# Kernel optimization log

Measured on AMD Instinct MI355X. Metric: run time of the kernel, lower is better.

## Reference

```python
import jax, jax.numpy as jnp
import numpy as np

EPS_BN = 1e-5
EPS_ATTN = 1e-9


def bn(h, g, b, m, v):
    # inference-mode BatchNorm1d over channel (last) dim
    return (h - m) * (g * jax.lax.rsqrt(v + EPS_BN)) + b


def setup_inputs() -> dict:
    key = jax.random.key(0)
    ks = jax.random.split(key, 16)
    B, N, Cin, C = 16, 2048, 64, 256
    std = 0.05
    inp = {
        "x": jax.random.normal(ks[0], (B, N, Cin), jnp.float32),
        "w1": jax.random.normal(ks[1], (C, Cin), jnp.float32) * std,
        "w2": jax.random.normal(ks[2], (C, C), jnp.float32) * std,
        "wqk": jax.random.normal(ks[3], (C, C), jnp.float32) * std,
        "wv": jax.random.normal(ks[4], (C, C), jnp.float32) * std,
        "bv": jax.random.normal(ks[5], (C,), jnp.float32) * std,
        "wt": jax.random.normal(ks[6], (C, C), jnp.float32) * std,
        "bt": jax.random.normal(ks[7], (C,), jnp.float32) * std,
    }
    for i, name in enumerate(["bn1", "bn2", "bn3"]):
        k = jax.random.split(ks[8 + i], 4)
        inp[name + "_g"] = 1.0 + 0.1 * jax.random.normal(k[0], (C,), jnp.float32)
        inp[name + "_b"] = 0.1 * jax.random.normal(k[1], (C,), jnp.float32)
        inp[name + "_m"] = 0.1 * jax.random.normal(k[2], (C,), jnp.float32)
        inp[name + "_v"] = jax.random.uniform(k[3], (C,), jnp.float32, 0.5, 1.5)
    return inp


def reference(x, w1, w2, wqk, wv, bv, wt, bt,
              bn1_g, bn1_b, bn1_m, bn1_v,
              bn2_g, bn2_b, bn2_m, bn2_v,
              bn3_g, bn3_b, bn3_m, bn3_v):
    # x: [B, N, Cin]; all feature maps kept channel-last [B, N, C]
    h = jax.nn.relu(bn(jnp.einsum('bnc,dc->bnd', x, w1), bn1_g, bn1_b, bn1_m, bn1_v))
    h = jax.nn.relu(bn(jnp.einsum('bnc,dc->bnd', h, w2), bn2_g, bn2_b, bn2_m, bn2_v))

    # SA_Layer: q and k share the same (bias-free) 1x1 conv weights
    q = jnp.einsum('bnc,dc->bnd', h, wqk)          # [B,N,C]
    energy = jnp.einsum('bic,bjc->bij', q, q)      # [B,N,N]
    attn = jax.nn.softmax(energy, axis=-1)
    attn = attn / (EPS_ATTN + jnp.sum(attn, axis=1, keepdims=True))  # L1 renorm over queries
    v = jnp.einsum('bnc,dc->bnd', h, wv) + bv      # [B,N,C]
    x_r = jnp.einsum('bic,bij->bjc', v, attn)      # [B,N,C]

    t = jnp.einsum('bnc,dc->bnd', h - x_r, wt) + bt
    t = jax.nn.relu(bn(t, bn3_g, bn3_b, bn3_m, bn3_v))
    out = h + t                                    # [B,N,C]
    return jnp.transpose(out, (0, 2, 1))           # [B,C,N] as in torch module
```

## Files before the change

### kernel.cpp

```cpp
#include <hip/hip_runtime.h>
#include <hip/hip_bf16.h>

#define B_  16
#define N_  2048
#define C_  256
#define BN_ (B_*N_)

typedef __bf16 bf16x8 __attribute__((ext_vector_type(8)));
typedef float  f32x4  __attribute__((ext_vector_type(4)));
typedef int    i32x4  __attribute__((ext_vector_type(4)));

static __device__ __forceinline__ f32x4 MFMA(bf16x8 a, bf16x8 b, f32x4 c){
  return __builtin_amdgcn_mfma_f32_16x16x32_bf16(a, b, c, 0, 0, 0);
}
static __device__ __forceinline__ unsigned short f2b(float f){
  unsigned int u = __float_as_uint(f);
  u += 0x7fffu + ((u >> 16) & 1u);
  return (unsigned short)(u >> 16);
}

__global__ void prep_kernel(
    const float* __restrict__ w1, const float* __restrict__ w2,
    const float* __restrict__ wqk, const float* __restrict__ wv,
    const float* __restrict__ bv, const float* __restrict__ wt,
    const float* __restrict__ bt,
    const float* __restrict__ g1, const float* __restrict__ b1,
    const float* __restrict__ m1, const float* __restrict__ v1,
    const float* __restrict__ g2, const float* __restrict__ b2,
    const float* __restrict__ m2, const float* __restrict__ v2,
    const float* __restrict__ g3, const float* __restrict__ b3,
    const float* __restrict__ m3, const float* __restrict__ v3,
    unsigned short* __restrict__ w1b, unsigned short* __restrict__ w2b,
    unsigned short* __restrict__ wqkb, unsigned short* __restrict__ wvb,
    unsigned short* __restrict__ wtb,
    float* __restrict__ bias1, float* __restrict__ bias2,
    float* __restrict__ biasv, float* __restrict__ biast)
{
  const int d = blockIdx.x;
  const int c = threadIdx.x;
  const float s1 = g1[d] * rsqrtf(v1[d] + 1e-5f);
  const float s2 = g2[d] * rsqrtf(v2[d] + 1e-5f);
  const float s3 = g3[d] * rsqrtf(v3[d] + 1e-5f);
  if (c < 64) w1b[d*64 + c] = f2b(w1[d*64 + c] * s1);
  w2b[d*256 + c]  = f2b(w2[d*256 + c] * s2);
  wqkb[d*256 + c] = f2b(wqk[d*256 + c]);
  wvb[d*256 + c]  = f2b(wv[d*256 + c]);
  wtb[d*256 + c]  = f2b(wt[d*256 + c] * s3);
  if (c == 0){
    bias1[d] = b1[d] - m1[d]*s1;
    bias2[d] = b2[d] - m2[d]*s2;
    biasv[d] = bv[d];
    biast[d] = bt[d]*s3 + b3[d] - m3[d]*s3;
  }
}

template<int MODE, int K>
__global__ __launch_bounds__(256, 2) void wgemm(
    const void* __restrict__ inp, const unsigned short* __restrict__ wB,
    const float* __restrict__ bias, const float* __restrict__ hf32,
    void* __restrict__ out0, void* __restrict__ out1)
{
  extern __shared__ char smem[];
  unsigned short* Al = (unsigned short*)smem;
  unsigned short* Bl = (unsigned short*)(smem + 64*72*2);
  const int tid  = threadIdx.x;
  const int lane = tid & 63;
  const int w    = tid >> 6;
  const int wr   = w >> 1, wc = w & 1;
  const long row0 = (long)blockIdx.x * 64;

  f32x4 acc[2][8];
  #pragma unroll
  for (int m = 0; m < 2; ++m)
    #pragma unroll
    for (int n = 0; n < 8; ++n) acc[m][n] = f32x4{0.f,0.f,0.f,0.f};

  const int KS = K / 64;
  #pragma unroll 1
  for (int s = 0; s < KS; ++s){
    if (s) __syncthreads();
    if constexpr (MODE == 0){
      const float* xin = (const float*)inp;
      #pragma unroll
      for (int t = 0; t < 4; ++t){
        int idx = tid + t*256;
        int r = idx >> 4, c4 = (idx & 15) * 4;
        float4 v = *(const float4*)(xin + (row0 + r)*K + c4);
        unsigned short* dst = &Al[r*72 + c4];
        dst[0]=f2b(v.x); dst[1]=f2b(v.y); dst[2]=f2b(v.z); dst[3]=f2b(v.w);
      }
    } else {
      const unsigned short* bin = (const unsigned short*)inp;
      #pragma unroll
      for (int t = 0; t < 2; ++t){
        int idx = tid + t*256;
        int r = idx >> 3, c8 = (idx & 7) * 8;
        *(i32x4*)&Al[r*72 + c8] = *(const i32x4*)(bin + (row0 + r)*K + s*64 + c8);
      }
    }
    #pragma unroll
    for (int t = 0; t < 8; ++t){
      int idx = tid + t*256;
      int d = idx >> 3, c8 = (idx & 7) * 8;
      *(i32x4*)&Bl[d*72 + c8] = *(const i32x4*)(wB + d*K + s*64 + c8);
    }
    __syncthreads();
    #pragma unroll
    for (int kk = 0; kk < 2; ++kk){
      bf16x8 a[2], b[8];
      #pragma unroll
      for (int m = 0; m < 2; ++m)
        a[m] = *(const bf16x8*)&Al[(32*wr + 16*m + (lane&15))*72 + kk*32 + (lane>>4)*8];
      #pragma unroll
      for (int n = 0; n < 8; ++n)
        b[n] = *(const bf16x8*)&Bl[(128*wc + 16*n + (lane&15))*72 + kk*32 + (lane>>4)*8];
      #pragma unroll
      for (int m = 0; m < 2; ++m)
        #pragma unroll
        for (int n = 0; n < 8; ++n)
          acc[m][n] = MFMA(a[m], b[n], acc[m][n]);
    }
  }

  if constexpr (MODE <= 2){
    unsigned short* obf = (unsigned short*)out0;
    float* of = (float*)out1;
    #pragma unroll
    for (int n = 0; n < 8; ++n){
      int col = 128*wc + 16*n + (lane&15);
      float bs = 0.f;
      if constexpr (MODE != 2) bs = bias[col];
      #pragma unroll
      for (int m = 0; m < 2; ++m){
        int rl = 32*wr + 16*m + (lane>>4)*4;
        #pragma unroll
        for (int r = 0; r < 4; ++r){
          float v = acc[m][n][r] + bs;
          if constexpr (MODE == 0 || MODE == 1) v = fmaxf(v, 0.f);
          obf[(row0 + rl + r)*256 + col] = f2b(v);
          if constexpr (MODE == 1) of[(row0 + rl + r)*256 + col] = v;
        }
      }
    }
  } else if constexpr (MODE == 3){
    __syncthreads();
    unsigned short* Vl = (unsigned short*)smem;
    #pragma unroll
    for (int n = 0; n < 8; ++n){
      int col = 128*wc + 16*n + (lane&15);
      float bs = bias[col];
      #pragma unroll
      for (int m = 0; m < 2; ++m){
        int rl = 32*wr + 16*m + (lane>>4)*4;
        #pragma unroll
        for (int r = 0; r < 4; ++r)
          Vl[(rl + r)*264 + col] = f2b(acc[m][n][r] + bs);
      }
    }
    __syncthreads();
    long b = row0 >> 11;
    int  n0 = (int)(row0 & 2047);
    unsigned short* vt = (unsigned short*)out0 + b*(256L*2048);
    #pragma unroll 1
    for (int cc = 0; cc < 64; ++cc){
      int c = 64*w + cc;
      vt[(long)c*2048 + n0 + lane] = Vl[lane*264 + c];
    }
  } else {
    __syncthreads();
    float* Ol = (float*)smem;
    #pragma unroll
    for (int n = 0; n < 8; ++n){
      int col = 128*wc + 16*n + (lane&15);
      float bs = bias[col];
      #pragma unroll
      for (int m = 0; m < 2; ++m){
        int rl = 32*wr + 16*m + (lane>>4)*4;
        #pragma unroll
        for (int r = 0; r < 4; ++r){
          float t = fmaxf(acc[m][n][r] + bs, 0.f);
          float h = hf32[(row0 + rl + r)*256 + col];
          Ol[(rl + r)*265 + col] = h + t;
        }
      }
    }
    __syncthreads();
    long b = row0 >> 11;
    int  n0 = (int)(row0 & 2047);
    float* op = (float*)out0 + b*(256L*2048);
    #pragma unroll 1
    for (int cc = 0; cc < 64; ++cc){
      int c = 64*w + cc;
      op[(long)c*2048 + n0 + lane] = Ol[lane*265 + c];
    }
  }
}

__global__ __launch_bounds__(256, 2) void pass1_kernel(
    const unsigned short* __restrict__ q,
    float* __restrict__ rowm, float* __restrict__ rowl)
{
  __shared__ unsigned short qi[64*264];
  __shared__ float smm[4][64], sml[4][64];
  const int tid = threadIdx.x, lane = tid & 63, w = tid >> 6;
  const int lin = blockIdx.y * 32 + blockIdx.x;
  const int swz = (lin & 7) * 64 + (lin >> 3);
  const int b  = swz >> 5;
  const int i0 = (swz & 31) * 64;
  const unsigned short* qb = q + (long)b*N_*C_;

  #pragma unroll
  for (int t = 0; t < 8; ++t){
    int idx = tid + t*256;
    int r = idx >> 5, c8 = (idx & 31) * 8;
    *(i32x4*)&qi[r*264 + c8] = *(const i32x4*)(qb + (long)(i0 + r)*256 + c8);
  }
  __syncthreads();

  float mr[4][4], lr[4][4];
  #pragma unroll
  for (int i = 0; i < 4; ++i)
    #pragma unroll
    for (int r = 0; r < 4; ++r){ mr[i][r] = -3e38f; lr[i][r] = 0.f; }

  #pragma unroll 1
  for (int js = 0; js < 8; ++js){
    const int j0 = js*256 + 64*w;
    f32x4 e[4][4];
    #pragma unroll
    for (int i = 0; i < 4; ++i)
      #pragma unroll
      for (int j = 0; j < 4; ++j) e[i][j] = f32x4{0.f,0.f,0.f,0.f};

    #pragma unroll
    for (int kk = 0; kk < 8; ++kk){
      bf16x8 a[4], bb[4];
      #pragma unroll
      for (int i = 0; i < 4; ++i)
        a[i] = *(const bf16x8*)&qi[(16*i + (lane&15))*264 + kk*32 + (lane>>4)*8];
      #pragma unroll
      for (int j = 0; j < 4; ++j)
        bb[j] = *(const bf16x8*)(qb + (long)(j0 + 16*j + (lane&15))*256 + kk*32 + (lane>>4)*8);
      #pragma unroll
      for (int i = 0; i < 4; ++i)
        #pragma unroll
        for (int j = 0; j < 4; ++j)
          e[i][j] = MFMA(a[i], bb[j], e[i][j]);
    }
    #pragma unroll
    for (int i = 0; i < 4; ++i)
      #pragma unroll
      for (int r = 0; r < 4; ++r){
        float tm = fmaxf(fmaxf(e[i][0][r], e[i][1][r]), fmaxf(e[i][2][r], e[i][3][r]));
        tm = fmaxf(tm, __shfl_xor(tm, 1));
        tm = fmaxf(tm, __shfl_xor(tm, 2));
        tm = fmaxf(tm, __shfl_xor(tm, 4));
        tm = fmaxf(tm, __shfl_xor(tm, 8));
        float mn = fmaxf(mr[i][r], tm);
        float p = __expf(e[i][0][r]-mn) + __expf(e[i][1][r]-mn)
                + __expf(e[i][2][r]-mn) + __expf(e[i][3][r]-mn);
        p += __shfl_xor(p, 1); p += __shfl_xor(p, 2);
        p += __shfl_xor(p, 4); p += __shfl_xor(p, 8);
        lr[i][r] = lr[i][r]*__expf(mr[i][r]-mn) + p;
        mr[i][r] = mn;
      }
  }

  if ((lane & 15) == 0){
    #pragma unroll
    for (int i = 0; i < 4; ++i)
      #pragma unroll
      for (int r = 0; r < 4; ++r){
        int rl = 16*i + (lane>>4)*4 + r;
        smm[w][rl] = mr[i][r];
        sml[w][rl] = lr[i][r];
      }
  }
  __syncthreads();
  if (tid < 64){
    float m0 = smm[0][tid], m1 = smm[1][tid], m2 = smm[2][tid], m3 = smm[3][tid];
    float M = fmaxf(fmaxf(m0, m1), fmaxf(m2, m3));
    float L = sml[0][tid]*__expf(m0 - M) + sml[1][tid]*__expf(m1 - M)
            + sml[2][tid]*__expf(m2 - M) + sml[3][tid]*__expf(m3 - M);
    rowm[(long)b*N_ + i0 + tid] = M;
    rowl[(long)b*N_ + i0 + tid] = L;
  }
}

__global__ __launch_bounds__(256, 2) void pass2_kernel(
    const unsigned short* __restrict__ q, const unsigned short* __restrict__ vT,
    const float* __restrict__ rowm, const float* __restrict__ rowl,
    const float* __restrict__ hf, unsigned short* __restrict__ dbf)
{
  extern __shared__ char smem[];
  unsigned short* qj = (unsigned short*)smem;
  unsigned short* pl = qj + 64*264;
  float* colsum = (float*)(pl + 64*264);
  const int tid = threadIdx.x, lane = tid & 63, w = tid >> 6;
  const int lin = blockIdx.y * 32 + blockIdx.x;
  const int swz = (lin & 7) * 64 + (lin >> 3);
  const int b  = swz >> 5;
  const int j0 = (swz & 31) * 64;
  const unsigned short* qb = q  + (long)b*N_*C_;
  const unsigned short* vb = vT + (long)b*N_*C_;
  const float* mrow = rowm + (long)b*N_;
  const float* lrow = rowl + (long)b*N_;

  #pragma unroll
  for (int t = 0; t < 8; ++t){
    int idx = tid + t*256;
    int r = idx >> 5, c8 = (idx & 31) * 8;
    *(i32x4*)&qj[r*264 + c8] = *(const i32x4*)(qb + (long)(j0 + r)*256 + c8);
  }
  if (tid < 64) colsum[tid] = 0.f;
  __syncthreads();

  float cs[4][4];
  #pragma unroll
  for (int a = 0; a < 4; ++a)
    #pragma unroll
    for (int r = 0; r < 4; ++r) cs[a][r] = 0.f;
  f32x4 nm[4][4];
  #pragma unroll
  for (int a = 0; a < 4; ++a)
    #pragma unroll
    for (int c = 0; c < 4; ++c) nm[a][c] = f32x4{0.f,0.f,0.f,0.f};

  unsigned int pk[4][4][2];

  #pragma unroll 1
  for (int is = 0; is < 8; ++is){
    const int i0 = is * 256;
    const int iw = i0 + 64*w;

    float mi[4], ri[4];
    #pragma unroll
    for (int f = 0; f < 4; ++f){
      int ig = iw + 16*f + (lane&15);
      mi[f] = mrow[ig];
      ri[f] = __builtin_amdgcn_rcpf(lrow[ig]);
    }

    f32x4 e[4][4];
    #pragma unroll
    for (int a = 0; a < 4; ++a)
      #pragma unroll
      for (int f = 0; f < 4; ++f) e[a][f] = f32x4{0.f,0.f,0.f,0.f};
    #pragma unroll
    for (int kk = 0; kk < 8; ++kk){
      bf16x8 a[4], bb[4];
      #pragma unroll
      for (int jf = 0; jf < 4; ++jf)
        a[jf] = *(const bf16x8*)&qj[(16*jf + (lane&15))*264 + kk*32 + (lane>>4)*8];
      #pragma unroll
      for (int f = 0; f < 4; ++f)
        bb[f] = *(const bf16x8*)(qb + (long)(iw + 16*f + (lane&15))*256 + kk*32 + (lane>>4)*8);
      #pragma unroll
      for (int jf = 0; jf < 4; ++jf)
        #pragma unroll
        for (int f = 0; f < 4; ++f)
          e[jf][f] = MFMA(a[jf], bb[f], e[jf][f]);
    }

    if (is > 0){
      const int ip = i0 - 256;
      #pragma unroll
      for (int kc = 0; kc < 8; ++kc){
        bf16x8 pa[4], vv[4];
        #pragma unroll
        for (int jf = 0; jf < 4; ++jf)
          pa[jf] = *(const bf16x8*)&pl[(16*jf + (lane&15))*264 + kc*32 + (lane>>4)*8];
        #pragma unroll
        for (int cf = 0; cf < 4; ++cf)
          vv[cf] = *(const bf16x8*)(vb + (long)(64*w + 16*cf + (lane&15))*2048 + ip + kc*32 + (lane>>4)*8);
        #pragma unroll
        for (int jf = 0; jf < 4; ++jf)
          #pragma unroll
          for (int cf = 0; cf < 4; ++cf)
            nm[jf][cf] = MFMA(pa[jf], vv[cf], nm[jf][cf]);
      }
    }

    #pragma unroll
    for (int f = 0; f < 4; ++f){
      #pragma unroll
      for (int jf = 0; jf < 4; ++jf){
        #pragma unroll
        for (int rp = 0; rp < 2; ++rp){
          float p0 = __expf(e[jf][f][2*rp]   - mi[f]) * ri[f];
          float p1 = __expf(e[jf][f][2*rp+1] - mi[f]) * ri[f];
          cs[jf][2*rp]   += p0;
          cs[jf][2*rp+1] += p1;
          pk[jf][f][rp] = (unsigned int)f2b(p0) | ((unsigned int)f2b(p1) << 16);
        }
      }
    }

    __syncthreads();
    #pragma unroll
    for (int jf = 0; jf < 4; ++jf)
      #pragma unroll
      for (int f = 0; f < 4; ++f)
        #pragma unroll
        for (int rp = 0; rp < 2; ++rp){
          unsigned int v = pk[jf][f][rp];
          int col = 64*w + 16*f + (lane&15);
          pl[(16*jf + (lane>>4)*4 + 2*rp)*264 + col]     = (unsigned short)v;
          pl[(16*jf + (lane>>4)*4 + 2*rp+1)*264 + col]   = (unsigned short)(v >> 16);
        }
    __syncthreads();
  }

  {
    const int ip = 7 * 256;
    #pragma unroll
    for (int kc = 0; kc < 8; ++kc){
      bf16x8 pa[4], vv[4];
      #pragma unroll
      for (int jf = 0; jf < 4; ++jf)
        pa[jf] = *(const bf16x8*)&pl[(16*jf + (lane&15))*264 + kc*32 + (lane>>4)*8];
      #pragma unroll
      for (int cf = 0; cf < 4; ++cf)
        vv[cf] = *(const bf16x8*)(vb + (long)(64*w + 16*cf + (lane&15))*2048 + ip + kc*32 + (lane>>4)*8);
      #pragma unroll
      for (int jf = 0; jf < 4; ++jf)
        #pragma unroll
        for (int cf = 0; cf < 4; ++cf)
          nm[jf][cf] = MFMA(pa[jf], vv[cf], nm[jf][cf]);
    }
  }

  #pragma unroll
  for (int jf = 0; jf < 4; ++jf)
    #pragma unroll
    for (int r = 0; r < 4; ++r){
      float v = cs[jf][r];
      v += __shfl_xor(v, 1); v += __shfl_xor(v, 2);
      v += __shfl_xor(v, 4); v += __shfl_xor(v, 8);
      if ((lane & 15) == 0) atomicAdd(&colsum[16*jf + (lane>>4)*4 + r], v);
    }
  __syncthreads();

  #pragma unroll
  for (int jf = 0; jf < 4; ++jf)
    #pragma unroll
    for (int r = 0; r < 4; ++r){
      int jl = 16*jf + (lane>>4)*4 + r;
      float rcs = __builtin_amdgcn_rcpf(1e-9f + colsum[jl]);
      long rowg = (long)b*N_ + j0 + jl;
      #pragma unroll
      for (int cf = 0; cf < 4; ++cf){
        int c = 64*w + 16*cf + (lane&15);
        float xr = nm[jf][cf][r] * rcs;
        float d = hf[rowg*256 + c] - xr;
        dbf[rowg*256 + c] = f2b(d);
      }
    }
}

extern "C" void kernel_launch(void* const* d_in, const int* in_sizes, int n_in,
                              void* d_out, int out_size, void* d_ws, size_t ws_size,
                              hipStream_t stream)
{
  const float* x   = (const float*)d_in[0];
  const float* w1  = (const float*)d_in[1];
  const float* w2  = (const float*)d_in[2];
  const float* wqk = (const float*)d_in[3];
  const float* wv  = (const float*)d_in[4];
  const float* bv  = (const float*)d_in[5];
  const float* wt  = (const float*)d_in[6];
  const float* bt  = (const float*)d_in[7];
  const float* g1 = (const float*)d_in[8],  *b1 = (const float*)d_in[9];
  const float* m1 = (const float*)d_in[10], *v1 = (const float*)d_in[11];
  const float* g2 = (const float*)d_in[12], *b2 = (const float*)d_in[13];
  const float* m2 = (const float*)d_in[14], *v2 = (const float*)d_in[15];
  const float* g3 = (const float*)d_in[16], *b3 = (const float*)d_in[17];
  const float* m3 = (const float*)d_in[18], *v3 = (const float*)d_in[19];

  char* ws = (char*)d_ws;
  size_t off = 0;
  auto alloc = [&](size_t bytes)->char*{
    char* p = ws + off; off += (bytes + 255) & ~(size_t)255; return p;
  };
  unsigned short* w1b  = (unsigned short*)alloc(256*64*2);
  unsigned short* w2b  = (unsigned short*)alloc(256*256*2);
  unsigned short* wqkb = (unsigned short*)alloc(256*256*2);
  unsigned short* wvb  = (unsigned short*)alloc(256*256*2);
  unsigned short* wtb  = (unsigned short*)alloc(256*256*2);
  float* bias1 = (float*)alloc(256*4);
  float* bias2 = (float*)alloc(256*4);
  float* biasv = (float*)alloc(256*4);
  float* biast = (float*)alloc(256*4);
  unsigned short* h1_bf = (unsigned short*)alloc((size_t)BN_*C_*2);
  float*          h_f32 = (float*)alloc((size_t)BN_*C_*4);
  unsigned short* h_bf  = (unsigned short*)alloc((size_t)BN_*C_*2);
  unsigned short* q_bf  = (unsigned short*)alloc((size_t)BN_*C_*2);
  unsigned short* vT_bf = (unsigned short*)alloc((size_t)BN_*C_*2);
  float* rowm = (float*)alloc((size_t)BN_*4);
  float* rowl = (float*)alloc((size_t)BN_*4);
  unsigned short* d_bf  = (unsigned short*)alloc((size_t)BN_*C_*2);
  (void)ws_size; (void)in_sizes; (void)n_in; (void)out_size;

  hipFuncSetAttribute((const void*)&pass2_kernel,
                      hipFuncAttributeMaxDynamicSharedMemorySize, 67840);
  hipFuncSetAttribute((const void*)&wgemm<4,256>,
                      hipFuncAttributeMaxDynamicSharedMemorySize, 67840);

  prep_kernel<<<256, 256, 0, stream>>>(w1, w2, wqk, wv, bv, wt, bt,
      g1,b1,m1,v1, g2,b2,m2,v2, g3,b3,m3,v3,
      w1b, w2b, wqkb, wvb, wtb, bias1, bias2, biasv, biast);

  wgemm<0,64><<<512, 256, 46080, stream>>>(x, w1b, bias1, nullptr, h1_bf, nullptr);
  wgemm<1,256><<<512, 256, 46080, stream>>>(h1_bf, w2b, bias2, nullptr, h_bf, h_f32);
  wgemm<2,256><<<512, 256, 46080, stream>>>(h_bf, wqkb, nullptr, nullptr, q_bf, nullptr);
  wgemm<3,256><<<512, 256, 46080, stream>>>(h_bf, wvb, biasv, nullptr, vT_bf, nullptr);

  pass1_kernel<<<dim3(32,16), 256, 0, stream>>>(q_bf, rowm, rowl);
  pass2_kernel<<<dim3(32,16), 256, 67840, stream>>>(q_bf, vT_bf, rowm, rowl, h_f32, d_bf);

  wgemm<4,256><<<512, 256, 67840, stream>>>(d_bf, wtb, biast, h_f32, d_out, nullptr);
}
```

Measured before the change: 391.7 us.

## Transpose MFMA operands in pass1 and double-buffer fragment loads

In the softmax statistics pass, the MFMA operand order is swapped so each lane holds a query row's energies along the accumulator's register dimension. The running max and sum are then kept per lane without a shuffle reduction at every step, and lanes are combined only once at the end with two xor shuffles. Fragment loads from LDS and global memory for the next k-slice are double-buffered so they can overlap with the current MFMAs. The costs are higher register pressure from the two buffers and more exp calls per lane.

New measurement: 361.7 us. 1.08x faster.

```diff
diff --git a/kernel.cpp b/kernel.cpp
--- a/kernel.cpp
+++ b/kernel.cpp
@@ -203,6 +203,7 @@
   __shared__ unsigned short qi[64*264];
   __shared__ float smm[4][64], sml[4][64];
   const int tid = threadIdx.x, lane = tid & 63, w = tid >> 6;
+  const int l15 = lane & 15, hi = lane >> 4;
   const int lin = blockIdx.y * 32 + blockIdx.x;
   const int swz = (lin & 7) * 64 + (lin >> 3);
   const int b  = swz >> 5;
@@ -217,64 +218,76 @@
   }
   __syncthreads();
 
-  float mr[4][4], lr[4][4];
-  #pragma unroll
-  for (int i = 0; i < 4; ++i)
-    #pragma unroll
-    for (int r = 0; r < 4; ++r){ mr[i][r] = -3e38f; lr[i][r] = 0.f; }
+  float mloc[4], lloc[4];
+  #pragma unroll
+  for (int ii = 0; ii < 4; ++ii){ mloc[ii] = -3e38f; lloc[ii] = 0.f; }
 
   #pragma unroll 1
   for (int js = 0; js < 8; ++js){
     const int j0 = js*256 + 64*w;
     f32x4 e[4][4];
     #pragma unroll
-    for (int i = 0; i < 4; ++i)
-      #pragma unroll
-      for (int j = 0; j < 4; ++j) e[i][j] = f32x4{0.f,0.f,0.f,0.f};
+    for (int jf = 0; jf < 4; ++jf)
+      #pragma unroll
+      for (int ii = 0; ii < 4; ++ii) e[jf][ii] = f32x4{0.f,0.f,0.f,0.f};
+
+    bf16x8 aa[2][4], bb[2][4];
+    #pragma unroll
+    for (int ii = 0; ii < 4; ++ii)
+      aa[0][ii] = *(const bf16x8*)&qi[(16*ii + l15)*264 + hi*8];
+    #pragma unroll
+    for (int jf = 0; jf < 4; ++jf)
+      bb[0][jf] = *(const bf16x8*)(qb + (long)(j0 + 16*jf + l15)*256 + hi*8);
 
     #pragma unroll
     for (int kk = 0; kk < 8; ++kk){
-      bf16x8 a[4], bb[4];
-      #pragma unroll
-      for (int i = 0; i < 4; ++i)
-        a[i] = *(const bf16x8*)&qi[(16*i + (lane&15))*264 + kk*32 + (lane>>4)*8];
-      #pragma unroll
-      for (int j = 0; j < 4; ++j)
-        bb[j] = *(const bf16x8*)(qb + (long)(j0 + 16*j + (lane&15))*256 + kk*32 + (lane>>4)*8);
-      #pragma unroll
-      for (int i = 0; i < 4; ++i)
-        #pragma unroll
-        for (int j = 0; j < 4; ++j)
-          e[i][j] = MFMA(a[i], bb[j], e[i][j]);
-    }
-    #pragma unroll
-    for (int i = 0; i < 4; ++i)
-      #pragma unroll
-      for (int r = 0; r < 4; ++r){
-        float tm = fmaxf(fmaxf(e[i][0][r], e[i][1][r]), fmaxf(e[i][2][r], e[i][3][r]));
-        tm = fmaxf(tm, __shfl_xor(tm, 1));
-        tm = fmaxf(tm, __shfl_xor(tm, 2));
-        tm = fmaxf(tm, __shfl_xor(tm, 4));
-        tm = fmaxf(tm, __shfl_xor(tm, 8));
-        float mn = fmaxf(mr[i][r], tm);
-        float p = __expf(e[i][0][r]-mn) + __expf(e[i][1][r]-mn)
-                + __expf(e[i][2][r]-mn) + __expf(e[i][3][r]-mn);
-        p += __shfl_xor(p, 1); p += __shfl_xor(p, 2);
-        p += __shfl_xor(p, 4); p += __shfl_xor(p, 8);
-        lr[i][r] = lr[i][r]*__expf(mr[i][r]-mn) + p;
-        mr[i][r] = mn;
-      }
-  }
-
-  if ((lane & 15) == 0){
-    #pragma unroll
-    for (int i = 0; i < 4; ++i)
-      #pragma unroll
-      for (int r = 0; r < 4; ++r){
-        int rl = 16*i + (lane>>4)*4 + r;
-        smm[w][rl] = mr[i][r];
-        sml[w][rl] = lr[i][r];
-      }
+      const int cur = kk & 1, nxt = cur ^ 1;
+      if (kk < 7){
+        #pragma unroll
+        for (int ii = 0; ii < 4; ++ii)
+          aa[nxt][ii] = *(const bf16x8*)&qi[(16*ii + l15)*264 + (kk+1)*32 + hi*8];
+        #pragma unroll
+        for (int jf = 0; jf < 4; ++jf)
+          bb[nxt][jf] = *(const bf16x8*)(qb + (long)(j0 + 16*jf + l15)*256 + (kk+1)*32 + hi*8);
+      }
+      #pragma unroll
+      for (int jf = 0; jf < 4; ++jf)
+        #pragma unroll
+        for (int ii = 0; ii < 4; ++ii)
+          e[jf][ii] = MFMA(bb[cur][jf], aa[cur][ii], e[jf][ii]);
+    }
+
+    #pragma unroll
+    for (int ii = 0; ii < 4; ++ii){
+      float tm = fmaxf(fmaxf(fmaxf(e[0][ii][0], e[0][ii][1]), fmaxf(e[0][ii][2], e[0][ii][3])),
+                       fmaxf(fmaxf(e[1][ii][0], e[1][ii][1]), fmaxf(e[1][ii][2], e[1][ii][3])));
+      tm = fmaxf(tm, fmaxf(fmaxf(fmaxf(e[2][ii][0], e[2][ii][1]), fmaxf(e[2][ii][2], e[2][ii][3])),
+                           fmaxf(fmaxf(e[3][ii][0], e[3][ii][1]), fmaxf(e[3][ii][2], e[3][ii][3]))));
+      float mn = fmaxf(mloc[ii], tm);
+      float p = 0.f;
+      #pragma unroll
+      for (int jf = 0; jf < 4; ++jf)
+        #pragma unroll
+        for (int r = 0; r < 4; ++r)
+          p += __expf(e[jf][ii][r] - mn);
+      lloc[ii] = lloc[ii]*__expf(mloc[ii] - mn) + p;
+      mloc[ii] = mn;
+    }
+  }
+
+  #pragma unroll
+  for (int ii = 0; ii < 4; ++ii){
+    float m0 = mloc[ii], l0 = lloc[ii];
+    float mo = __shfl_xor(m0, 16), lo = __shfl_xor(l0, 16);
+    float mn = fmaxf(m0, mo);
+    l0 = l0*__expf(m0 - mn) + lo*__expf(mo - mn); m0 = mn;
+    mo = __shfl_xor(m0, 32); lo = __shfl_xor(l0, 32);
+    mn = fmaxf(m0, mo);
+    l0 = l0*__expf(m0 - mn) + lo*__expf(mo - mn); m0 = mn;
+    if (lane < 16){
+      smm[w][16*ii + l15] = m0;
+      sml[w][16*ii + l15] = l0;
+    }
   }
   __syncthreads();
   if (tid < 64){
```
